# Kernel optimization log

Hardware: AMD Instinct MI355X
Metric: run time of the kernel (lower is better)

## Reference

```python
import jax, jax.numpy as jnp
import numpy as np

B, C, H, W = 8, 320, 64, 64      # query feature map
S_KV, D_KV = 77, 1024            # key/value (text) tokens
HEADS, DIM_HEAD = 8, 64
INNER = HEADS * DIM_HEAD         # 512


def setup_inputs() -> dict:
    key = jax.random.key(0)
    ks = jax.random.split(key, 7)
    return {
        "query": jax.random.normal(ks[0], (B, C, H, W), dtype=jnp.float32),
        "key_value": jax.random.normal(ks[1], (B, S_KV, D_KV), dtype=jnp.float32),
        "Wq": jax.random.normal(ks[2], (C, INNER), dtype=jnp.float32) * (C ** -0.5),
        "Wk": jax.random.normal(ks[3], (D_KV, INNER), dtype=jnp.float32) * (D_KV ** -0.5),
        "Wv": jax.random.normal(ks[4], (D_KV, INNER), dtype=jnp.float32) * (D_KV ** -0.5),
        "Wo": jax.random.normal(ks[5], (INNER, C), dtype=jnp.float32) * (INNER ** -0.5),
        "bo": jnp.zeros((C,), dtype=jnp.float32),
    }


def reference(query, key_value, Wq, Wk, Wv, Wo, bo):
    b, c, h, w = query.shape
    n = h * w
    # [B,C,H,W] -> [B,N,C]
    q_flat = query.reshape(b, c, n).transpose(0, 2, 1)
    # projections, then split heads: [B, S, heads, dim_head]
    q = (q_flat @ Wq).reshape(b, n, HEADS, DIM_HEAD)
    k = (key_value @ Wk).reshape(b, S_KV, HEADS, DIM_HEAD)
    v = (key_value @ Wv).reshape(b, S_KV, HEADS, DIM_HEAD)
    scale = DIM_HEAD ** -0.5
    # attn logits: [B, heads, N, S_kv]
    logits = jnp.einsum('bnhd,bshd->bhns', q, k) * scale
    attn = jax.nn.softmax(logits, axis=-1)
    # weighted values -> merge heads: [B, N, inner]
    out = jnp.einsum('bhns,bshd->bnhd', attn, v).reshape(b, n, INNER)
    out = out @ Wo + bo  # dropout p=0.0 is identity
    # [B,N,C] -> [B,C,H,W]
    return out.transpose(0, 2, 1).reshape(b, c, h, w)
```

## Files before the change

### kernel.cpp

```cpp
#include <hip/hip_runtime.h>
#include <hip/hip_bf16.h>
#include <stdint.h>

#define BB     8
#define CC     320
#define NN     4096
#define SKV    77
#define HEADS  8
#define INNER  512
#define SCALE  0.125f

typedef float f32x4  __attribute__((ext_vector_type(4)));
typedef short bf16x8 __attribute__((ext_vector_type(8)));
typedef short s16x4  __attribute__((ext_vector_type(4)));

static __device__ __forceinline__ short f2bf(float f) {
  unsigned u = __float_as_uint(f);
  return (short)((u + 0x7fffu + ((u >> 16) & 1u)) >> 16);
}

static __device__ __forceinline__ void gll16(void* lds, const void* g) {
  auto gp = reinterpret_cast<const uint32_t __attribute__((address_space(1)))*>(
      reinterpret_cast<uintptr_t>(g));
  auto lp = reinterpret_cast<uint32_t __attribute__((address_space(3)))*>(
      reinterpret_cast<uintptr_t>(lds));
  __builtin_amdgcn_global_load_lds(gp, lp, 16, 0, 0);
}

__global__ __launch_bounds__(256) void prep_kernel(
    const float* __restrict__ kv, const float* __restrict__ Wk,
    const float* __restrict__ Wv, const float* __restrict__ Wq,
    const float* __restrict__ Wo, const float* __restrict__ query,
    short* __restrict__ kv_bf, short* __restrict__ Wk_t,
    short* __restrict__ Wv_t, short* __restrict__ Wq_t,
    short* __restrict__ Wo_t, short* __restrict__ X_bf,
    unsigned* __restrict__ zero_base) {
  __shared__ float T[64 * 65];
  const int blk = blockIdx.x, t = threadIdx.x;
  if (blk < 616) {
    const int base = blk * 1024;
    #pragma unroll
    for (int i = 0; i < 4; ++i) kv_bf[base + i*256 + t] = f2bf(kv[base + i*256 + t]);
    return;
  }
  if (blk >= 1208) {
    const int blk2 = blk - 1208;
    const int b = blk2 / 320, r = blk2 % 320;
    const int nt = r / 5, ct = r % 5;
    const int tl = t & 63, rb = t >> 6;
    #pragma unroll
    for (int i = 0; i < 16; ++i) {
      const int c = rb + i*4;
      T[c*65 + tl] = query[((size_t)(b*CC + ct*64 + c))*NN + nt*64 + tl];
    }
    __syncthreads();
    #pragma unroll
    for (int i = 0; i < 16; ++i) {
      const int n = rb + i*4;
      X_bf[((size_t)(b*NN + nt*64 + n))*CC + ct*64 + tl] = f2bf(T[tl*65 + n]);
    }
    return;
  }
  if (blk >= 952) {
    const int base = (blk - 952) * 1024;
    #pragma unroll
    for (int i = 0; i < 4; ++i) zero_base[base + i*256 + t] = 0u;
    return;
  }
  const float* src; short* dst; int RS, CS, kt, ct; float scl = 1.0f;
  if (blk < 872) {
    const int tile = blk - 616;
    const bool isK = tile < 128;
    const int tt = isK ? tile : tile - 128;
    src = isK ? Wk : Wv; dst = isK ? Wk_t : Wv_t;
    RS = 1024; CS = 512; kt = tt >> 3; ct = tt & 7;
  } else if (blk < 912) {
    const int tt = blk - 872;
    src = Wq; dst = Wq_t; RS = 320; CS = 512; kt = tt >> 3; ct = tt & 7;
    scl = SCALE;
  } else {
    const int tt = blk - 912;
    src = Wo; dst = Wo_t; RS = 512; CS = 320; kt = tt / 5; ct = tt % 5;
  }
  const int cl = t & 63, rb = t >> 6;
  #pragma unroll
  for (int i = 0; i < 16; ++i)
    T[(rb + i*4)*65 + cl] = src[(size_t)(kt*64 + rb + i*4)*CS + ct*64 + cl];
  __syncthreads();
  #pragma unroll
  for (int i = 0; i < 16; ++i) {
    const int nl = rb + i*4;
    dst[(size_t)(ct*64 + nl)*RS + kt*64 + cl] = f2bf(T[cl*65 + nl] * scl);
  }
}

__global__ __launch_bounds__(256) void kvproj_kernel(
    const short* __restrict__ kv_bf, const short* __restrict__ Wk_t,
    const short* __restrict__ Wv_t, short* __restrict__ K_ws,
    short* __restrict__ V_ws) {
  const int t = threadIdx.x, w = t >> 6, lane = t & 63;
  const int l15 = lane & 15, q = lane >> 4;
  const int m0 = (blockIdx.x * 4 + w) * 16;
  const int y = blockIdx.y;
  const bool isK = (y < 8);
  const int h = y & 7;
  const short* __restrict__ Wt = isK ? Wk_t : Wv_t;
  const int arow = (m0 + l15 < 616) ? (m0 + l15) : 615;

  const f32x4 z = {0.f, 0.f, 0.f, 0.f};
  f32x4 acc[4] = {z, z, z, z};
  for (int k0 = 0; k0 < 1024; k0 += 32) {
    const bf16x8 a = *(const bf16x8*)(kv_bf + (size_t)arow*1024 + k0 + q*8);
    #pragma unroll
    for (int nt = 0; nt < 4; ++nt) {
      const int n = h*64 + nt*16 + l15;
      const bf16x8 bfr = *(const bf16x8*)(Wt + (size_t)n*1024 + k0 + q*8);
      acc[nt] = __builtin_amdgcn_mfma_f32_16x16x32_bf16(a, bfr, acc[nt], 0, 0, 0);
    }
  }
  #pragma unroll
  for (int nt = 0; nt < 4; ++nt) {
    const int d = nt*16 + l15;
    #pragma unroll
    for (int r = 0; r < 4; ++r) {
      const int row = m0 + q*4 + r;
      if (row < 616) {
        const int b = (int)(((unsigned)row * 54472u) >> 22);
        const int s = row - b*77;
        if (isK) {
          const int u = (d >> 3) ^ (s & 7);
          K_ws[(size_t)((b*8 + h)*80 + s)*64 + u*8 + (d & 7)] = f2bf(acc[nt][r]);
        } else {
          const int u = (s >> 3) ^ (d & 15);
          V_ws[(size_t)((b*8 + h)*64 + d)*128 + u*8 + (s & 7)] = f2bf(acc[nt][r]);
        }
      }
    }
  }
}

__global__ __launch_bounds__(256, 2) void qproj_kernel(
    const short* __restrict__ X_bf, const short* __restrict__ Wq_t,
    short* __restrict__ Q_ws) {
  const int t = threadIdx.x, w = t >> 6, lane = t & 63;
  const int l15 = lane & 15, q = lane >> 4;
  const int m0 = (blockIdx.x >> 1) * 128;
  const int n0 = (blockIdx.x & 1) * 256;
  const int wm = w & 1, wn = w >> 1;

  __shared__ short tile[2][12288];

  auto stage = [&](int it, int bufi) {
    short* buf = tile[bufi];
    const int k0 = it * 32;
    #pragma unroll
    for (int p = 0; p < 2; ++p) {
      const int f = p*256 + t, row = f >> 2, c4 = f & 3;
      const int c4s = c4 ^ ((row & 3) ^ ((row >> 2) & 3));
      gll16(buf + f*8, X_bf + (size_t)(m0 + row)*320 + k0 + c4s*8);
    }
    #pragma unroll
    for (int p = 0; p < 4; ++p) {
      const int f = p*256 + t, row = f >> 2, c4 = f & 3;
      const int c4s = c4 ^ ((row & 3) ^ ((row >> 2) & 3));
      gll16(buf + 4096 + f*8, Wq_t + (size_t)(n0 + row)*320 + k0 + c4s*8);
    }
  };

  const f32x4 z = {0.f, 0.f, 0.f, 0.f};
  f32x4 acc[4][8];
  #pragma unroll
  for (int mt = 0; mt < 4; ++mt)
    #pragma unroll
    for (int nt = 0; nt < 8; ++nt) acc[mt][nt] = z;

  stage(0, 0);
  __syncthreads();
  const int lperm = (l15 & 3) ^ ((l15 >> 2) & 3);
  for (int it = 0; it < 10; ++it) {
    if (it + 1 < 10) stage(it + 1, (it + 1) & 1);
    const short* buf = tile[it & 1];
    bf16x8 a[4], bb[8];
    #pragma unroll
    for (int mt = 0; mt < 4; ++mt)
      a[mt] = *(const bf16x8*)(buf + (wm*64 + mt*16 + l15)*32 + (q ^ lperm)*8);
    #pragma unroll
    for (int nt = 0; nt < 8; ++nt)
      bb[nt] = *(const bf16x8*)(buf + 4096 + (wn*128 + nt*16 + l15)*32 + (q ^ lperm)*8);
    #pragma unroll
    for (int mt = 0; mt < 4; ++mt)
      #pragma unroll
      for (int nt = 0; nt < 8; ++nt)
        acc[mt][nt] = __builtin_amdgcn_mfma_f32_16x16x32_bf16(a[mt], bb[nt], acc[mt][nt], 0, 0, 0);
    if (it + 1 < 10) __syncthreads();
  }
  #pragma unroll
  for (int mt = 0; mt < 4; ++mt)
    #pragma unroll
    for (int r = 0; r < 4; ++r) {
      short* rowp = Q_ws + (size_t)(m0 + wm*64 + mt*16 + q*4 + r)*512 + n0 + wn*128;
      #pragma unroll
      for (int nt = 0; nt < 8; ++nt)
        rowp[nt*16 + l15] = f2bf(acc[mt][nt][r]);
    }
}

__global__ __launch_bounds__(256) void attncore_kernel(
    const short* __restrict__ Q_ws, const short* __restrict__ K_ws,
    const short* __restrict__ V_ws, short* __restrict__ O_ws) {
  const int t = threadIdx.x, w = t >> 6, lane = t & 63;
  const int l15 = lane & 15, q = lane >> 4;
  const int b = blockIdx.x >> 7;
  const int r7 = blockIdx.x & 127;
  const int h = r7 >> 4;
  const int rng = r7 & 15;

  __shared__ short KL[80 * 64];
  __shared__ short VL[64 * 128];
  __shared__ short scr[4 * 32 * 104];

  const short* __restrict__ Kg = K_ws + (size_t)(b*8 + h) * 80 * 64;
  const short* __restrict__ Vg = V_ws + (size_t)(b*8 + h) * 64 * 128;
  #pragma unroll
  for (int p = 0; p < 3; ++p) {
    const int L = p*256 + t;
    if (L < 640) gll16(KL + L*8, Kg + L*8);
  }
  #pragma unroll
  for (int p = 0; p < 4; ++p) {
    const int L = p*256 + t;
    gll16(VL + L*8, Vg + L*8);
  }
  short* scrw = scr + w * 3328;
  for (int i = lane; i < 1664; i += 64) ((unsigned*)scrw)[i] = 0u;
  __syncthreads();

  const f32x4 z = {0.f, 0.f, 0.f, 0.f};
  for (int chunk = 0; chunk < 2; ++chunk) {
    const int n0 = rng * 256 + w * 64 + chunk * 32;
    size_t tokrow[2];
    #pragma unroll
    for (int nt = 0; nt < 2; ++nt) tokrow[nt] = (size_t)(b*NN + n0 + nt*16 + l15);

    f32x4 qk[2][5];
    #pragma unroll
    for (int nt = 0; nt < 2; ++nt)
      #pragma unroll
      for (int st = 0; st < 5; ++st) qk[nt][st] = z;
    #pragma unroll
    for (int f = 0; f < 2; ++f) {
      bf16x8 bq[2];
      #pragma unroll
      for (int nt = 0; nt < 2; ++nt)
        bq[nt] = *(const bf16x8*)(Q_ws + tokrow[nt]*512 + h*64 + f*32 + q*8);
      #pragma unroll
      for (int st = 0; st < 5; ++st) {
        const int srow = st*16 + l15;
        const bf16x8 a = *(const bf16x8*)(KL + srow*64 + ((f*4 + q) ^ (srow & 7))*8);
        #pragma unroll
        for (int nt = 0; nt < 2; ++nt)
          qk[nt][st] = __builtin_amdgcn_mfma_f32_16x16x32_bf16(a, bq[nt], qk[nt][st], 0, 0, 0);
      }
    }

    #pragma unroll
    for (int nt = 0; nt < 2; ++nt) {
      float mx = -1e30f;
      #pragma unroll
      for (int st = 0; st < 5; ++st)
        #pragma unroll
        for (int r = 0; r < 4; ++r) {
          const int s = st*16 + q*4 + r;
          const float vv = (s < SKV) ? qk[nt][st][r] : -1e30f;
          qk[nt][st][r] = vv;
          mx = fmaxf(mx, vv);
        }
      mx = fmaxf(mx, __shfl_xor(mx, 16));
      mx = fmaxf(mx, __shfl_xor(mx, 32));
      float sum = 0.f;
      #pragma unroll
      for (int st = 0; st < 5; ++st)
        #pragma unroll
        for (int r = 0; r < 4; ++r) {
          const int s = st*16 + q*4 + r;
          const float e = (s < SKV) ? __expf(qk[nt][st][r] - mx) : 0.f;
          qk[nt][st][r] = e;
          sum += e;
        }
      sum += __shfl_xor(sum, 16);
      sum += __shfl_xor(sum, 32);
      const float inv = 1.0f / sum;
      #pragma unroll
      for (int st = 0; st < 5; ++st) {
        s16x4 pv;
        #pragma unroll
        for (int r = 0; r < 4; ++r) pv[r] = f2bf(qk[nt][st][r] * inv);
        *(s16x4*)(scrw + (nt*16 + l15)*104 + st*16 + q*4) = pv;
      }
    }

    f32x4 ov[2][4];
    #pragma unroll
    for (int nt = 0; nt < 2; ++nt)
      #pragma unroll
      for (int dt = 0; dt < 4; ++dt) ov[nt][dt] = z;
    #pragma unroll
    for (int f = 0; f < 3; ++f) {
      bf16x8 bp[2];
      #pragma unroll
      for (int nt = 0; nt < 2; ++nt)
        bp[nt] = *(const bf16x8*)(scrw + (nt*16 + l15)*104 + f*32 + q*8);
      #pragma unroll
      for (int dt = 0; dt < 4; ++dt) {
        const int vrow = dt*16 + l15;
        const bf16x8 a = *(const bf16x8*)(VL + vrow*128 + ((f*4 + q) ^ (vrow & 15))*8);
        #pragma unroll
        for (int nt = 0; nt < 2; ++nt)
          ov[nt][dt] = __builtin_amdgcn_mfma_f32_16x16x32_bf16(a, bp[nt], ov[nt][dt], 0, 0, 0);
      }
    }
    #pragma unroll
    for (int nt = 0; nt < 2; ++nt)
      #pragma unroll
      for (int dt = 0; dt < 4; ++dt) {
        s16x4 pv;
        #pragma unroll
        for (int r = 0; r < 4; ++r) pv[r] = f2bf(ov[nt][dt][r]);
        *(s16x4*)(O_ws + tokrow[nt]*512 + h*64 + dt*16 + q*4) = pv;
      }
  }
}

__global__ __launch_bounds__(256) void outproj_kernel(
    const short* __restrict__ O_ws, const short* __restrict__ Wo_t,
    const float* __restrict__ bo, float* __restrict__ out) {
  const int t = threadIdx.x, w = t >> 6, lane = t & 63;
  const int l15 = lane & 15, q = lane >> 4;
  const int c0 = (blockIdx.x & 1) * 160;
  const int t0 = (blockIdx.x >> 1) * 128;
  const int wm = w & 1, wn = w >> 1;

  __shared__ short tile[2][9216];

  auto stage = [&](int it, int bufi) {
    short* buf = tile[bufi];
    const int k0 = it * 32;
    #pragma unroll
    for (int p = 0; p < 5; ++p) {
      const int f = p*256 + t;
      if (f < 1152) {
        const short* g;
        if (f < 640) {
          const int row = f >> 2, c4 = f & 3;
          const int c4s = c4 ^ ((row & 3) ^ ((row >> 2) & 3));
          g = Wo_t + (size_t)(c0 + row)*512 + k0 + c4s*8;
        } else {
          const int f2 = f - 640, row = f2 >> 2, c4 = f2 & 3;
          const int c4s = c4 ^ ((row & 3) ^ ((row >> 2) & 3));
          g = O_ws + (size_t)(t0 + row)*512 + k0 + c4s*8;
        }
        gll16(buf + f*8, g);
      }
    }
  };

  const f32x4 z = {0.f, 0.f, 0.f, 0.f};
  f32x4 acc[5][4];
  #pragma unroll
  for (int mt = 0; mt < 5; ++mt)
    #pragma unroll
    for (int nt = 0; nt < 4; ++nt) acc[mt][nt] = z;

  stage(0, 0);
  __syncthreads();
  const int lperm = (l15 & 3) ^ ((l15 >> 2) & 3);
  for (int it = 0; it < 16; ++it) {
    if (it + 1 < 16) stage(it + 1, (it + 1) & 1);
    const short* buf = tile[it & 1];
    bf16x8 a[5], bb[4];
    #pragma unroll
    for (int mt = 0; mt < 5; ++mt)
      a[mt] = *(const bf16x8*)(buf + (wm*80 + mt*16 + l15)*32 + (q ^ lperm)*8);
    #pragma unroll
    for (int nt = 0; nt < 4; ++nt)
      bb[nt] = *(const bf16x8*)(buf + 5120 + (wn*64 + nt*16 + l15)*32 + (q ^ lperm)*8);
    #pragma unroll
    for (int mt = 0; mt < 5; ++mt)
      #pragma unroll
      for (int nt = 0; nt < 4; ++nt)
        acc[mt][nt] = __builtin_amdgcn_mfma_f32_16x16x32_bf16(a[mt], bb[nt], acc[mt][nt], 0, 0, 0);
    if (it + 1 < 16) __syncthreads();
  }
  const int b = t0 >> 12, n = t0 & 4095;
  #pragma unroll
  for (int mt = 0; mt < 5; ++mt)
    #pragma unroll
    for (int r = 0; r < 4; ++r) {
      const int c = c0 + wm*80 + mt*16 + q*4 + r;
      const float bv = bo[c];
      float* rowp = out + ((size_t)(b*CC + c))*NN + n + wn*64;
      #pragma unroll
      for (int nt = 0; nt < 4; ++nt)
        rowp[nt*16 + l15] = acc[mt][nt][r] + bv;
    }
}

extern "C" void kernel_launch(void* const* d_in, const int* in_sizes, int n_in,
                              void* d_out, int out_size, void* d_ws, size_t ws_size,
                              hipStream_t stream) {
  const float* query = (const float*)d_in[0];
  const float* kv    = (const float*)d_in[1];
  const float* Wq    = (const float*)d_in[2];
  const float* Wk    = (const float*)d_in[3];
  const float* Wv    = (const float*)d_in[4];
  const float* Wo    = (const float*)d_in[5];
  const float* bo    = (const float*)d_in[6];
  float* out = (float*)d_out;

  char* p = (char*)d_ws;
  short* K_ws  = (short*)(p);
  short* V_ws  = (short*)(p +   819200);
  short* Wq_t  = (short*)(p +  1867776);
  short* Wo_t  = (short*)(p +  2195456);
  short* kv_bf = (short*)(p +  2523136);
  short* Wk_t  = (short*)(p +  3784704);
  short* Wv_t  = (short*)(p +  4833280);
  short* X_bf  = (short*)(p +  5881856);
  short* Q_ws  = (short*)(p + 26853376);
  short* O_ws  = (short*)(p + 60407808);

  prep_kernel<<<3768, 256, 0, stream>>>(kv, Wk, Wv, Wq, Wo, query, kv_bf,
                                        Wk_t, Wv_t, Wq_t, Wo_t, X_bf,
                                        (unsigned*)V_ws);
  kvproj_kernel<<<dim3(10, 16), 256, 0, stream>>>(kv_bf, Wk_t, Wv_t, K_ws, V_ws);
  qproj_kernel<<<512, 256, 0, stream>>>(X_bf, Wq_t, Q_ws);
  attncore_kernel<<<1024, 256, 0, stream>>>(Q_ws, K_ws, V_ws, O_ws);
  outproj_kernel<<<512, 256, 0, stream>>>(O_ws, Wo_t, bo, out);
}
```

Before: 185.3 us.

## Fuse query transpose into Q projection and merge K/V/Q projection kernels

Removes the separate transpose-to-bf16 pass over the query tensor, which wrote an intermediate X_bf buffer. The Q projection now reads fp32 query directly, converting and transposing it into a padded LDS tile. The K/V projection is folded into the same launch as extra blocks, each now covering half a head, so the two run concurrently. This saves a full write and read of the activation intermediate and one launch, at the cost of larger LDS use and smaller Q tiles (64 rows), which mean more Wq reloads.

Result: no change. 184.1 us (-0.7%).

```diff
diff --git a/kernel.cpp b/kernel.cpp
--- a/kernel.cpp
+++ b/kernel.cpp
@@ -30,10 +30,9 @@
 __global__ __launch_bounds__(256) void prep_kernel(
     const float* __restrict__ kv, const float* __restrict__ Wk,
     const float* __restrict__ Wv, const float* __restrict__ Wq,
-    const float* __restrict__ Wo, const float* __restrict__ query,
-    short* __restrict__ kv_bf, short* __restrict__ Wk_t,
-    short* __restrict__ Wv_t, short* __restrict__ Wq_t,
-    short* __restrict__ Wo_t, short* __restrict__ X_bf,
+    const float* __restrict__ Wo, short* __restrict__ kv_bf,
+    short* __restrict__ Wk_t, short* __restrict__ Wv_t,
+    short* __restrict__ Wq_t, short* __restrict__ Wo_t,
     unsigned* __restrict__ zero_base) {
   __shared__ float T[64 * 65];
   const int blk = blockIdx.x, t = threadIdx.x;
@@ -41,24 +40,6 @@
     const int base = blk * 1024;
     #pragma unroll
     for (int i = 0; i < 4; ++i) kv_bf[base + i*256 + t] = f2bf(kv[base + i*256 + t]);
-    return;
-  }
-  if (blk >= 1208) {
-    const int blk2 = blk - 1208;
-    const int b = blk2 / 320, r = blk2 % 320;
-    const int nt = r / 5, ct = r % 5;
-    const int tl = t & 63, rb = t >> 6;
-    #pragma unroll
-    for (int i = 0; i < 16; ++i) {
-      const int c = rb + i*4;
-      T[c*65 + tl] = query[((size_t)(b*CC + ct*64 + c))*NN + nt*64 + tl];
-    }
-    __syncthreads();
-    #pragma unroll
-    for (int i = 0; i < 16; ++i) {
-      const int n = rb + i*4;
-      X_bf[((size_t)(b*NN + nt*64 + n))*CC + ct*64 + tl] = f2bf(T[tl*65 + n]);
-    }
     return;
   }
   if (blk >= 952) {
@@ -94,83 +75,95 @@
   }
 }
 
-__global__ __launch_bounds__(256) void kvproj_kernel(
+__global__ __launch_bounds__(256, 2) void proj_kernel(
+    const float* __restrict__ query, const short* __restrict__ Wq_t,
     const short* __restrict__ kv_bf, const short* __restrict__ Wk_t,
-    const short* __restrict__ Wv_t, short* __restrict__ K_ws,
-    short* __restrict__ V_ws) {
+    const short* __restrict__ Wv_t, short* __restrict__ Q_ws,
+    short* __restrict__ K_ws, short* __restrict__ V_ws) {
   const int t = threadIdx.x, w = t >> 6, lane = t & 63;
   const int l15 = lane & 15, q = lane >> 4;
-  const int m0 = (blockIdx.x * 4 + w) * 16;
-  const int y = blockIdx.y;
-  const bool isK = (y < 8);
-  const int h = y & 7;
-  const short* __restrict__ Wt = isK ? Wk_t : Wv_t;
-  const int arow = (m0 + l15 < 616) ? (m0 + l15) : 615;
-
-  const f32x4 z = {0.f, 0.f, 0.f, 0.f};
-  f32x4 acc[4] = {z, z, z, z};
-  for (int k0 = 0; k0 < 1024; k0 += 32) {
-    const bf16x8 a = *(const bf16x8*)(kv_bf + (size_t)arow*1024 + k0 + q*8);
-    #pragma unroll
-    for (int nt = 0; nt < 4; ++nt) {
-      const int n = h*64 + nt*16 + l15;
-      const bf16x8 bfr = *(const bf16x8*)(Wt + (size_t)n*1024 + k0 + q*8);
-      acc[nt] = __builtin_amdgcn_mfma_f32_16x16x32_bf16(a, bfr, acc[nt], 0, 0, 0);
-    }
-  }
-  #pragma unroll
-  for (int nt = 0; nt < 4; ++nt) {
-    const int d = nt*16 + l15;
-    #pragma unroll
-    for (int r = 0; r < 4; ++r) {
-      const int row = m0 + q*4 + r;
-      if (row < 616) {
-        const int b = (int)(((unsigned)row * 54472u) >> 22);
-        const int s = row - b*77;
-        if (isK) {
-          const int u = (d >> 3) ^ (s & 7);
-          K_ws[(size_t)((b*8 + h)*80 + s)*64 + u*8 + (d & 7)] = f2bf(acc[nt][r]);
-        } else {
-          const int u = (s >> 3) ^ (d & 15);
-          V_ws[(size_t)((b*8 + h)*64 + d)*128 + u*8 + (s & 7)] = f2bf(acc[nt][r]);
+
+  __shared__ short A[64 * 328];
+  __shared__ short Bt[2][8192];
+
+  if (blockIdx.x >= 1024) {
+    const int blk2 = blockIdx.x - 1024;
+    const int bx = blk2 % 10;
+    const int y  = blk2 / 10;
+    const bool isK = (y < 16);
+    const int yy = isK ? y : y - 16;
+    const int h = yy >> 1, dh = yy & 1;
+    const short* __restrict__ Wt = isK ? Wk_t : Wv_t;
+    const int m0 = (bx * 4 + w) * 16;
+    const int arow = (m0 + l15 < 616) ? (m0 + l15) : 615;
+
+    const f32x4 z = {0.f, 0.f, 0.f, 0.f};
+    f32x4 acc[2] = {z, z};
+    for (int k0 = 0; k0 < 1024; k0 += 32) {
+      const bf16x8 a = *(const bf16x8*)(kv_bf + (size_t)arow*1024 + k0 + q*8);
+      #pragma unroll
+      for (int nt = 0; nt < 2; ++nt) {
+        const int n = h*64 + dh*32 + nt*16 + l15;
+        const bf16x8 bfr = *(const bf16x8*)(Wt + (size_t)n*1024 + k0 + q*8);
+        acc[nt] = __builtin_amdgcn_mfma_f32_16x16x32_bf16(a, bfr, acc[nt], 0, 0, 0);
+      }
+    }
+    #pragma unroll
+    for (int nt = 0; nt < 2; ++nt) {
+      const int d = dh*32 + nt*16 + l15;
+      #pragma unroll
+      for (int r = 0; r < 4; ++r) {
+        const int row = m0 + q*4 + r;
+        if (row < 616) {
+          const int b = (int)(((unsigned)row * 54472u) >> 22);
+          const int s = row - b*77;
+          if (isK) {
+            const int u = (d >> 3) ^ (s & 7);
+            K_ws[(size_t)((b*8 + h)*80 + s)*64 + u*8 + (d & 7)] = f2bf(acc[nt][r]);
+          } else {
+            const int u = (s >> 3) ^ (d & 15);
+            V_ws[(size_t)((b*8 + h)*64 + d)*128 + u*8 + (s & 7)] = f2bf(acc[nt][r]);
+          }
         }
       }
     }
-  }
-}
-
-__global__ __launch_bounds__(256, 2) void qproj_kernel(
-    const short* __restrict__ X_bf, const short* __restrict__ Wq_t,
-    short* __restrict__ Q_ws) {
-  const int t = threadIdx.x, w = t >> 6, lane = t & 63;
-  const int l15 = lane & 15, q = lane >> 4;
-  const int m0 = (blockIdx.x >> 1) * 128;
-  const int n0 = (blockIdx.x & 1) * 256;
+    return;
+  }
+
+  const int g = blockIdx.x >> 1;
+  const int b = g >> 6;
+  const int n0 = (g & 63) * 64;
+  const int j0 = (blockIdx.x & 1) * 256;
   const int wm = w & 1, wn = w >> 1;
 
-  __shared__ short tile[2][12288];
+  {
+    const float* qb = query + (size_t)b * CC * NN + n0;
+    #pragma unroll
+    for (int i = 0; i < 20; ++i) {
+      const int f = i * 256 + t;
+      const int c = f >> 4, n4 = (f & 15) * 4;
+      const f32x4 v = *(const f32x4*)(qb + (size_t)c * NN + n4);
+      #pragma unroll
+      for (int j = 0; j < 4; ++j)
+        A[(n4 + j) * 328 + c] = f2bf(v[j]);
+    }
+  }
 
   auto stage = [&](int it, int bufi) {
-    short* buf = tile[bufi];
+    short* buf = Bt[bufi];
     const int k0 = it * 32;
-    #pragma unroll
-    for (int p = 0; p < 2; ++p) {
-      const int f = p*256 + t, row = f >> 2, c4 = f & 3;
-      const int c4s = c4 ^ ((row & 3) ^ ((row >> 2) & 3));
-      gll16(buf + f*8, X_bf + (size_t)(m0 + row)*320 + k0 + c4s*8);
-    }
     #pragma unroll
     for (int p = 0; p < 4; ++p) {
       const int f = p*256 + t, row = f >> 2, c4 = f & 3;
       const int c4s = c4 ^ ((row & 3) ^ ((row >> 2) & 3));
-      gll16(buf + 4096 + f*8, Wq_t + (size_t)(n0 + row)*320 + k0 + c4s*8);
+      gll16(buf + f*8, Wq_t + (size_t)(j0 + row)*320 + k0 + c4s*8);
     }
   };
 
   const f32x4 z = {0.f, 0.f, 0.f, 0.f};
-  f32x4 acc[4][8];
-  #pragma unroll
-  for (int mt = 0; mt < 4; ++mt)
+  f32x4 acc[2][8];
+  #pragma unroll
+  for (int mt = 0; mt < 2; ++mt)
     #pragma unroll
     for (int nt = 0; nt < 8; ++nt) acc[mt][nt] = z;
 
@@ -179,26 +172,27 @@
   const int lperm = (l15 & 3) ^ ((l15 >> 2) & 3);
   for (int it = 0; it < 10; ++it) {
     if (it + 1 < 10) stage(it + 1, (it + 1) & 1);
-    const short* buf = tile[it & 1];
-    bf16x8 a[4], bb[8];
-    #pragma unroll
-    for (int mt = 0; mt < 4; ++mt)
-      a[mt] = *(const bf16x8*)(buf + (wm*64 + mt*16 + l15)*32 + (q ^ lperm)*8);
+    const short* buf = Bt[it & 1];
+    const int k0 = it * 32;
+    bf16x8 a[2], bb[8];
+    #pragma unroll
+    for (int mt = 0; mt < 2; ++mt)
+      a[mt] = *(const bf16x8*)(A + (wm*32 + mt*16 + l15)*328 + k0 + q*8);
     #pragma unroll
     for (int nt = 0; nt < 8; ++nt)
-      bb[nt] = *(const bf16x8*)(buf + 4096 + (wn*128 + nt*16 + l15)*32 + (q ^ lperm)*8);
-    #pragma unroll
-    for (int mt = 0; mt < 4; ++mt)
+      bb[nt] = *(const bf16x8*)(buf + ((wn*128 + nt*16 + l15)*4 + (q ^ lperm))*8);
+    #pragma unroll
+    for (int mt = 0; mt < 2; ++mt)
       #pragma unroll
       for (int nt = 0; nt < 8; ++nt)
         acc[mt][nt] = __builtin_amdgcn_mfma_f32_16x16x32_bf16(a[mt], bb[nt], acc[mt][nt], 0, 0, 0);
     if (it + 1 < 10) __syncthreads();
   }
   #pragma unroll
-  for (int mt = 0; mt < 4; ++mt)
+  for (int mt = 0; mt < 2; ++mt)
     #pragma unroll
     for (int r = 0; r < 4; ++r) {
-      short* rowp = Q_ws + (size_t)(m0 + wm*64 + mt*16 + q*4 + r)*512 + n0 + wn*128;
+      short* rowp = Q_ws + (size_t)(b*NN + n0 + wm*32 + mt*16 + q*4 + r)*512 + j0 + wn*128;
       #pragma unroll
       for (int nt = 0; nt < 8; ++nt)
         rowp[nt*16 + l15] = f2bf(acc[mt][nt][r]);
@@ -380,10 +374,10 @@
     bf16x8 a[5], bb[4];
     #pragma unroll
     for (int mt = 0; mt < 5; ++mt)
-      a[mt] = *(const bf16x8*)(buf + (wm*80 + mt*16 + l15)*32 + (q ^ lperm)*8);
+      a[mt] = *(const bf16x8*)(buf + ((wm*80 + mt*16 + l15)*4 + (q ^ lperm))*8);
     #pragma unroll
     for (int nt = 0; nt < 4; ++nt)
-      bb[nt] = *(const bf16x8*)(buf + 5120 + (wn*64 + nt*16 + l15)*32 + (q ^ lperm)*8);
+      bb[nt] = *(const bf16x8*)(buf + 5120 + ((wn*64 + nt*16 + l15)*4 + (q ^ lperm))*8);
     #pragma unroll
     for (int mt = 0; mt < 5; ++mt)
       #pragma unroll
@@ -425,15 +419,14 @@
   short* kv_bf = (short*)(p +  2523136);
   short* Wk_t  = (short*)(p +  3784704);
   short* Wv_t  = (short*)(p +  4833280);
-  short* X_bf  = (short*)(p +  5881856);
-  short* Q_ws  = (short*)(p + 26853376);
-  short* O_ws  = (short*)(p + 60407808);
-
-  prep_kernel<<<3768, 256, 0, stream>>>(kv, Wk, Wv, Wq, Wo, query, kv_bf,
-                                        Wk_t, Wv_t, Wq_t, Wo_t, X_bf,
+  short* Q_ws  = (short*)(p +  5881856);
+  short* O_ws  = (short*)(p + 39436288);
+
+  prep_kernel<<<1208, 256, 0, stream>>>(kv, Wk, Wv, Wq, Wo, kv_bf,
+                                        Wk_t, Wv_t, Wq_t, Wo_t,
                                         (unsigned*)V_ws);
-  kvproj_kernel<<<dim3(10, 16), 256, 0, stream>>>(kv_bf, Wk_t, Wv_t, K_ws, V_ws);
-  qproj_kernel<<<512, 256, 0, stream>>>(X_bf, Wq_t, Q_ws);
+  proj_kernel<<<1344, 256, 0, stream>>>(query, Wq_t, kv_bf, Wk_t, Wv_t,
+                                        Q_ws, K_ws, V_ws);
   attncore_kernel<<<1024, 256, 0, stream>>>(Q_ws, K_ws, V_ws, O_ws);
   outproj_kernel<<<512, 256, 0, stream>>>(O_ws, Wo_t, bo, out);
 }
```
